# Kernel optimization log

Hardware: AMD Instinct MI355X
Metric: run time of the kernel (lower is better)

## Reference

```python
import jax, jax.numpy as jnp
import numpy as np

N, H, S, D = 2, 8, 2048, 64

def setup_inputs() -> dict:
    key = jax.random.key(0)
    k1, k2, k3, k4 = jax.random.split(key, 4)
    queries = jax.random.normal(k1, (N, H, S, D), dtype=jnp.float32)
    keys = jax.random.normal(k2, (N, H, S, D), dtype=jnp.float32)
    values = jax.random.normal(k3, (N, H, S, D), dtype=jnp.float32)
    attn_mask = jax.random.randint(k4, (1, 1, S, S), 0, 2, dtype=jnp.int32)
    return {"queries": queries, "keys": keys, "values": values, "attn_mask": attn_mask}

def reference(queries, keys, values, attn_mask):
    # Faithful to the torch code: softmax over axis=2 (query/seq axis) for Q,
    # softmax over axis=1 (heads axis) for K, exactly as written.
    Q = jax.nn.softmax(queries, axis=2)
    K = jax.nn.softmax(keys, axis=1)
    attention_weights = jnp.einsum('nhqd,nhkd->nhqk', Q, K)  # [N,H,S,S]
    attention_weights = jnp.where(attn_mask == 0, -jnp.inf, attention_weights)
    attention_weights = jax.nn.softmax(attention_weights, axis=-1)
    context = jnp.einsum('nhqk,nhkd->nhqd', attention_weights, values)
    return context, attention_weights
```

## Files before the change

### kernel.cpp

```cpp
#include <hip/hip_runtime.h>

#define S 2048
#define Dh 64
#define NH 16
#define SD (S*Dh)
#define SSZ ((size_t)S*(size_t)S)

typedef __attribute__((ext_vector_type(4))) float f32x4;
typedef __attribute__((ext_vector_type(8))) short s16x8;

#define WSB_QSUM 0
#define WSB_RINV 4096
#define WSB_MASK 135168
#define WSB_QS   659456
#define WSB_KS   (WSB_QS + 4194304)
#define WSB_VT   (WSB_KS + 4194304)

__device__ __forceinline__ ushort f2bf(float x) {
    unsigned u = __builtin_bit_cast(unsigned, x);
    u = (u + 0x7fffu + ((u >> 16) & 1u)) >> 16;
    return (ushort)u;
}

__device__ __forceinline__ void gload_lds16(const ushort* g, ushort* l) {
    __builtin_amdgcn_global_load_lds(
        (const __attribute__((address_space(1))) unsigned int*)(const void*)g,
        (__attribute__((address_space(3))) unsigned int*)(void*)l,
        16, 0, 0);
}

__global__ void k_qsum(const float* __restrict__ q, float* __restrict__ qsum) {
    const int head  = blockIdx.x >> 5;
    const int chunk = blockIdx.x & 31;
    const int t = threadIdx.x;
    const int d = t & 63, sg = t >> 6;
    const float* qh = q + (size_t)head * SD;
    const int s0 = chunk * 64;
    float acc = 0.f;
#pragma unroll
    for (int i = 0; i < 16; ++i) {
        int s = s0 + sg + 4 * i;
        acc += __expf(qh[s * Dh + d]);
    }
    __shared__ float part[4][64];
    part[sg][d] = acc;
    __syncthreads();
    if (sg == 0)
        atomicAdd(&qsum[head * 64 + d], part[0][d] + part[1][d] + part[2][d] + part[3][d]);
}

__global__ void k_qnorm(const float* __restrict__ q, const float* __restrict__ qsum,
                        ushort* __restrict__ Qs) {
    const int gid = blockIdx.x * 256 + threadIdx.x;
    const int i0 = gid * 8;
    const int head = i0 >> 17;
    const int d0 = i0 & 63;
    const float4 a = ((const float4*)(q + i0))[0];
    const float4 b = ((const float4*)(q + i0))[1];
    const float* qs = qsum + head * 64 + d0;
    s16x8 o;
    o[0] = (short)f2bf(__expf(a.x) / qs[0]);
    o[1] = (short)f2bf(__expf(a.y) / qs[1]);
    o[2] = (short)f2bf(__expf(a.z) / qs[2]);
    o[3] = (short)f2bf(__expf(a.w) / qs[3]);
    o[4] = (short)f2bf(__expf(b.x) / qs[4]);
    o[5] = (short)f2bf(__expf(b.y) / qs[5]);
    o[6] = (short)f2bf(__expf(b.z) / qs[6]);
    o[7] = (short)f2bf(__expf(b.w) / qs[7]);
    *(s16x8*)(Qs + i0) = o;
}

__global__ void k_ksoft(const float* __restrict__ kin, ushort* __restrict__ Ks) {
    const int gid = blockIdx.x * 256 + threadIdx.x;
    const int n = gid >> 17;
    const int rem = gid & (SD - 1);
    const float* base = kin + (size_t)n * 8 * SD + rem;
    float x[8];
    float sum = 0.f;
#pragma unroll
    for (int h = 0; h < 8; ++h) { x[h] = __expf(base[(size_t)h * SD]); sum += x[h]; }
    const float inv = 1.f / sum;
    ushort* ob = Ks + (size_t)n * 8 * SD + rem;
#pragma unroll
    for (int h = 0; h < 8; ++h) ob[(size_t)h * SD] = f2bf(x[h] * inv);
}

__global__ void k_vt(const float* __restrict__ V, ushort* __restrict__ Vt) {
    const int head = blockIdx.x >> 5, kt = blockIdx.x & 31;
    const int t = threadIdx.x;
    __shared__ float sv[64 * 68];
    const float4* src = (const float4*)(V + (size_t)head * SD + (size_t)kt * 64 * 64);
#pragma unroll
    for (int i = 0; i < 4; ++i) {
        int idx = t + 256 * i;
        int row = idx >> 4, c4 = idx & 15;
        *(float4*)&sv[row * 68 + c4 * 4] = src[idx];
    }
    __syncthreads();
    const int d = t >> 2, seg = t & 3;
    s16x8 v0, v1;
#pragma unroll
    for (int j = 0; j < 8; ++j) v0[j] = (short)f2bf(sv[(seg * 16 + j) * 68 + d]);
#pragma unroll
    for (int j = 0; j < 8; ++j) v1[j] = (short)f2bf(sv[(seg * 16 + 8 + j) * 68 + d]);
    ushort* dst = Vt + (size_t)head * SD + (size_t)d * S + kt * 64 + seg * 16;
    *(s16x8*)dst = v0;
    *(s16x8*)(dst + 8) = v1;
}

__global__ void k_mask(const int* __restrict__ mask, unsigned long long* __restrict__ bmt) {
    const int t = threadIdx.x;
    const int g = blockIdx.x * 4 + (t >> 6);
    const int lane = t & 63;
#pragma unroll
    for (int it = 0; it < 16; ++it) {
        int w = g * 16 + it;
        int m = mask[(size_t)w * 64 + lane];
        unsigned long long b = __ballot(m != 0);
        if (lane == 0) bmt[(size_t)(w & 31) * S + (w >> 5)] = b;
    }
}

__global__ __launch_bounds__(256, 4) void k_ctx(
        const ushort* __restrict__ Qs, const ushort* __restrict__ Ks,
        const ushort* __restrict__ Vt, const unsigned long long* __restrict__ bmt,
        float* __restrict__ ctx, float* __restrict__ rinv) {
    const int head = blockIdx.x, qt = blockIdx.y;
    const int q0 = qt * 32;
    const int t = threadIdx.x;
    const int lane = t & 63, w = t >> 6;
    const int wq = w & 1, kh = w >> 1;
    const int lm = lane & 15, lg = lane >> 4;
    const int q = q0 + 16 * wq + lm;

    __shared__ __align__(16) char smem[21760];
    ushort* sK = (ushort*)smem;
    ushort* sV = (ushort*)(smem + 8192);
    ushort* Pl = (ushort*)(smem + 16384);
    float*  redrs = (float*)(smem + 21504);
    float*  redo  = (float*)smem;

    const ushort* Qb = Qs + (size_t)head * SD;
    const ushort* Kb = Ks + (size_t)head * SD;
    const ushort* Vb = Vt + (size_t)head * SD;

    s16x8 bq[2];
#pragma unroll
    for (int h = 0; h < 2; ++h)
        bq[h] = *(const s16x8*)(Qb + (size_t)q * 64 + 32 * h + 8 * lg);

    f32x4 o[4];
#pragma unroll
    for (int dj = 0; dj < 4; ++dj) o[dj] = (f32x4){0.f, 0.f, 0.f, 0.f};
    float rs = 0.f;
    uint* prow = (uint*)&Pl[(w * 16 + lm) * 40];

    for (int kt = 0; kt < 32; ++kt) {
        const int k0 = kt * 64;
        __syncthreads();
#pragma unroll
        for (int i = 0; i < 2; ++i) {
            const int idx = t + 256 * i;
            const int row = idx >> 3, seg = idx & 7;
            const int sw = (seg ^ (row & 7)) * 8;
            gload_lds16(Kb + (size_t)(k0 + row) * 64 + sw, &sK[idx * 8]);
            gload_lds16(Vb + (size_t)row * S + k0 + sw, &sV[idx * 8]);
        }
        __syncthreads();

        f32x4 sc[2];
        sc[0] = (f32x4){0.f, 0.f, 0.f, 0.f};
        sc[1] = (f32x4){0.f, 0.f, 0.f, 0.f};
#pragma unroll
        for (int h = 0; h < 2; ++h)
#pragma unroll
            for (int jj = 0; jj < 2; ++jj) {
                const int row = 16 * (2 * kh + jj) + lm;
                s16x8 ak = *(const s16x8*)&sK[row * 64 + (((4 * h + lg) ^ (lm & 7)) * 8)];
                sc[jj] = __builtin_amdgcn_mfma_f32_16x16x32_bf16(ak, bq[h], sc[jj], 0, 0, 0);
            }
        const unsigned long long m64 = bmt[(size_t)kt * S + q];
        float rsum = 0.f;
#pragma unroll
        for (int jj = 0; jj < 2; ++jj)
#pragma unroll
            for (int p = 0; p < 2; ++p) {
                const int kloc = 16 * jj + 4 * lg + 2 * p;
                const int kbit = 32 * kh + kloc;
                const float e0 = ((m64 >> kbit) & 1ULL) ? __expf(sc[jj][2 * p]) : 0.f;
                const float e1 = ((m64 >> (kbit + 1)) & 1ULL) ? __expf(sc[jj][2 * p + 1]) : 0.f;
                rsum += e0 + e1;
                prow[kloc >> 1] = ((uint)f2bf(e1) << 16) | (uint)f2bf(e0);
            }
        rsum += __shfl_xor(rsum, 16);
        rsum += __shfl_xor(rsum, 32);
        rs += rsum;

        const s16x8 pb = *(const s16x8*)&Pl[(w * 16 + lm) * 40 + 8 * lg];
#pragma unroll
        for (int dj = 0; dj < 4; ++dj) {
            const int vrow = 16 * dj + lm;
            s16x8 av = *(const s16x8*)&sV[vrow * 64 + (((4 * kh + lg) ^ (lm & 7)) * 8)];
            o[dj] = __builtin_amdgcn_mfma_f32_16x16x32_bf16(av, pb, o[dj], 0, 0, 0);
        }
    }

    __syncthreads();
    if (kh == 1) {
        float* dst = redo + (wq * 64 + lane) * 20;
#pragma unroll
        for (int dj = 0; dj < 4; ++dj) *(f32x4*)&dst[dj * 4] = o[dj];
        if (lg == 0) redrs[wq * 16 + lm] = rs;
    }
    __syncthreads();
    if (kh == 0) {
        const float inv = 1.f / (rs + redrs[wq * 16 + lm]);
        if (lg == 0) rinv[head * S + q] = inv;
        const float* src = redo + (wq * 64 + lane) * 20;
        float* cb = ctx + (size_t)head * SD + (size_t)q * 64;
#pragma unroll
        for (int dj = 0; dj < 4; ++dj) {
            f32x4 oo = (o[dj] + *(const f32x4*)&src[dj * 4]) * inv;
            *(f32x4*)(cb + 16 * dj + 4 * lg) = oo;
        }
    }
}

__global__ __launch_bounds__(256, 6) void k_awrite(
        const ushort* __restrict__ Qs, const ushort* __restrict__ Ks,
        const unsigned long long* __restrict__ bmt, const float* __restrict__ rinv,
        float* __restrict__ A) {
    const int head = blockIdx.x, qt = blockIdx.y, kc = blockIdx.z;
    const int q0 = qt * 64;
    const int t = threadIdx.x;
    const int lane = t & 63, wv = t >> 6;
    const int lm = lane & 15, lg = lane >> 4;
    const int q = q0 + 16 * wv + lm;

    __shared__ __align__(16) ushort sK[64 * 64];

    const ushort* Qb = Qs + (size_t)head * SD;
    const ushort* Kb = Ks + (size_t)head * SD;
    float* Aq = A + (size_t)head * SSZ + (size_t)q * S;

    s16x8 bq[2];
#pragma unroll
    for (int h = 0; h < 2; ++h)
        bq[h] = *(const s16x8*)(Qb + (size_t)q * 64 + 32 * h + 8 * lg);
    const float invr = rinv[head * S + q];

    for (int kt8 = 0; kt8 < 8; ++kt8) {
        const int k0 = kc * 512 + kt8 * 64;
        __syncthreads();
#pragma unroll
        for (int i = 0; i < 2; ++i) {
            const int idx = t + 256 * i;
            const int row = idx >> 3, seg = idx & 7;
            gload_lds16(Kb + (size_t)(k0 + row) * 64 + ((seg ^ (row & 7)) * 8), &sK[idx * 8]);
        }
        __syncthreads();

        f32x4 sc[4];
#pragma unroll
        for (int j = 0; j < 4; ++j) sc[j] = (f32x4){0.f, 0.f, 0.f, 0.f};
#pragma unroll
        for (int h = 0; h < 2; ++h)
#pragma unroll
            for (int j = 0; j < 4; ++j) {
                s16x8 ak = *(const s16x8*)&sK[(16 * j + lm) * 64 + (((4 * h + lg) ^ (lm & 7)) * 8)];
                sc[j] = __builtin_amdgcn_mfma_f32_16x16x32_bf16(ak, bq[h], sc[j], 0, 0, 0);
            }
        const unsigned long long m64 = bmt[(size_t)(k0 >> 6) * S + q];
#pragma unroll
        for (int j = 0; j < 4; ++j) {
            f32x4 pv;
#pragma unroll
            for (int r = 0; r < 4; ++r) {
                const int b = 16 * j + 4 * lg + r;
                pv[r] = ((m64 >> b) & 1ULL) ? __expf(sc[j][r]) * invr : 0.f;
            }
            __builtin_nontemporal_store(pv, (f32x4*)&Aq[k0 + 16 * j + 4 * lg]);
        }
    }
}

extern "C" void kernel_launch(void* const* d_in, const int* in_sizes, int n_in,
                              void* d_out, int out_size, void* d_ws, size_t ws_size,
                              hipStream_t stream) {
    const float* q = (const float*)d_in[0];
    const float* k = (const float*)d_in[1];
    const float* v = (const float*)d_in[2];
    const int* mask = (const int*)d_in[3];
    float* out = (float*)d_out;
    char* ws = (char*)d_ws;

    float* qsum = (float*)(ws + WSB_QSUM);
    float* rinv = (float*)(ws + WSB_RINV);
    unsigned long long* bm = (unsigned long long*)(ws + WSB_MASK);
    ushort* Qs = (ushort*)(ws + WSB_QS);
    ushort* Ks = (ushort*)(ws + WSB_KS);
    ushort* Vt = (ushort*)(ws + WSB_VT);

    (void)hipMemsetAsync(d_ws, 0, 4096, stream);
    k_qsum<<<512, 256, 0, stream>>>(q, qsum);
    k_mask<<<1024, 256, 0, stream>>>(mask, bm);
    k_qnorm<<<1024, 256, 0, stream>>>(q, qsum, Qs);
    k_ksoft<<<1024, 256, 0, stream>>>(k, Ks);
    k_vt<<<512, 256, 0, stream>>>(v, Vt);
    k_ctx<<<dim3(16, 64), 256, 0, stream>>>(Qs, Ks, Vt, bm, out, rinv);
    k_awrite<<<dim3(16, 32, 4), 256, 0, stream>>>(Qs, Ks, bm, rinv, out + (size_t)NH * SD);
}
```

Measured before the change: 420.7 us.

## Double-buffer K tiles and stage attention rows through LDS for coalesced stores

The attention-weight writer now double-buffers the K tile in shared memory and prefetches the next tile and its mask word while computing the current one, cutting the barrier pair per iteration to a single barrier. Output probabilities are first written to a padded per-wave LDS scratch, then reread so each group of 16 lanes stores a contiguous 256-byte row segment, replacing scattered 16-byte stores. Launch bounds drop from 6 to 4 blocks per CU to fit the larger shared memory footprint, which may reduce occupancy for this store-bound kernel.

Result: faster. 383.4 us (-8.9%).

```diff
diff --git a/kernel.cpp b/kernel.cpp
--- a/kernel.cpp
+++ b/kernel.cpp
@@ -226,7 +226,7 @@
     }
 }
 
-__global__ __launch_bounds__(256, 6) void k_awrite(
+__global__ __launch_bounds__(256, 4) void k_awrite(
         const ushort* __restrict__ Qs, const ushort* __restrict__ Ks,
         const unsigned long long* __restrict__ bmt, const float* __restrict__ rinv,
         float* __restrict__ A) {
@@ -237,28 +237,41 @@
     const int lm = lane & 15, lg = lane >> 4;
     const int q = q0 + 16 * wv + lm;
 
-    __shared__ __align__(16) ushort sK[64 * 64];
+    __shared__ __align__(16) char smem[33792];
+    ushort* sK = (ushort*)smem;
+    float* sP = (float*)(smem + 16384);
 
     const ushort* Qb = Qs + (size_t)head * SD;
     const ushort* Kb = Ks + (size_t)head * SD;
-    float* Aq = A + (size_t)head * SSZ + (size_t)q * S;
+    float* Ah = A + (size_t)head * SSZ;
+
+    auto stage = [&](int b, int k0) {
+#pragma unroll
+        for (int i = 0; i < 2; ++i) {
+            const int idx = t + 256 * i;
+            const int row = idx >> 3, seg = idx & 7;
+            gload_lds16(Kb + (size_t)(k0 + row) * 64 + ((seg ^ (row & 7)) * 8),
+                        &sK[b * 4096 + idx * 8]);
+        }
+    };
 
     s16x8 bq[2];
 #pragma unroll
     for (int h = 0; h < 2; ++h)
         bq[h] = *(const s16x8*)(Qb + (size_t)q * 64 + 32 * h + 8 * lg);
     const float invr = rinv[head * S + q];
+    float* sPw = &sP[wv * 16 * 68];
+
+    stage(0, kc * 512);
+    unsigned long long m64 = bmt[(size_t)(kc * 8) * S + q];
+    __syncthreads();
 
     for (int kt8 = 0; kt8 < 8; ++kt8) {
         const int k0 = kc * 512 + kt8 * 64;
-        __syncthreads();
-#pragma unroll
-        for (int i = 0; i < 2; ++i) {
-            const int idx = t + 256 * i;
-            const int row = idx >> 3, seg = idx & 7;
-            gload_lds16(Kb + (size_t)(k0 + row) * 64 + ((seg ^ (row & 7)) * 8), &sK[idx * 8]);
-        }
-        __syncthreads();
+        const int cur = kt8 & 1;
+        if (kt8 < 7) stage(cur ^ 1, k0 + 64);
+        const unsigned long long m64n =
+            (kt8 < 7) ? bmt[(size_t)((k0 >> 6) + 1) * S + q] : 0ULL;
 
         f32x4 sc[4];
 #pragma unroll
@@ -267,10 +280,11 @@
         for (int h = 0; h < 2; ++h)
 #pragma unroll
             for (int j = 0; j < 4; ++j) {
-                s16x8 ak = *(const s16x8*)&sK[(16 * j + lm) * 64 + (((4 * h + lg) ^ (lm & 7)) * 8)];
+                s16x8 ak = *(const s16x8*)&sK[cur * 4096 + (16 * j + lm) * 64 +
+                                              (((4 * h + lg) ^ (lm & 7)) * 8)];
                 sc[j] = __builtin_amdgcn_mfma_f32_16x16x32_bf16(ak, bq[h], sc[j], 0, 0, 0);
             }
-        const unsigned long long m64 = bmt[(size_t)(k0 >> 6) * S + q];
+
 #pragma unroll
         for (int j = 0; j < 4; ++j) {
             f32x4 pv;
@@ -279,8 +293,17 @@
                 const int b = 16 * j + 4 * lg + r;
                 pv[r] = ((m64 >> b) & 1ULL) ? __expf(sc[j][r]) * invr : 0.f;
             }
-            __builtin_nontemporal_store(pv, (f32x4*)&Aq[k0 + 16 * j + 4 * lg]);
-        }
+            *(f32x4*)&sPw[lm * 68 + 16 * j + 4 * lg] = pv;
+        }
+#pragma unroll
+        for (int pass = 0; pass < 4; ++pass) {
+            const int rr = (lane >> 4) + 4 * pass;
+            f32x4 pv = *(const f32x4*)&sPw[rr * 68 + (lane & 15) * 4];
+            __builtin_nontemporal_store(pv,
+                (f32x4*)&Ah[(size_t)(q0 + 16 * wv + rr) * S + k0 + (lane & 15) * 4]);
+        }
+        __syncthreads();
+        m64 = m64n;
     }
 }
 
```
